# Performance work log

Measured on AMD Instinct MI355X. Metric: run time of the kernel, lower is better.

Reference implementation:

```python
import jax, jax.numpy as jnp
import numpy as np

B, S, D, F, E, K = 4, 2048, 1024, 4096, 8, 2
LBW = 0.01  # load_balance_weight


def setup_inputs() -> dict:
    key = jax.random.key(0)
    ks = jax.random.split(key, 8)
    sd, sf = 1.0 / np.sqrt(D), 1.0 / np.sqrt(F)
    return {
        "x": jax.random.normal(ks[0], (B, S, D), dtype=jnp.float32),
        "expert_weights": jax.random.normal(ks[1], (B, E), dtype=jnp.float32),
        "gate_w": jax.random.uniform(ks[2], (D, E), minval=-sd, maxval=sd),
        "gate_b": jnp.zeros((E,), jnp.float32),
        "w1": jax.random.uniform(ks[3], (E, D, F), minval=-sd, maxval=sd),
        "b1": jnp.zeros((E, F), jnp.float32),
        "w2": jax.random.uniform(ks[4], (E, F, D), minval=-sf, maxval=sf),
        "b2": jnp.zeros((E, D), jnp.float32),
    }


def reference(x, expert_weights, gate_w, gate_b, w1, b1, w2, b2):
    b, s, d = x.shape
    xf = x.reshape(-1, d)                       # (T, D), T = B*S
    T = xf.shape[0]

    logits = xf @ gate_w + gate_b               # (T, E)
    bias = jnp.broadcast_to(expert_weights[:, None, :], (b, s, E)).reshape(-1, E)
    gate_probs = jax.nn.softmax(logits + bias, axis=-1)

    topk_p, topk_i = jax.lax.top_k(gate_probs, K)
    topk_p = topk_p / topk_p.sum(axis=-1, keepdims=True)

    # combine[t, e] = renormalized routing weight of token t for expert e (0 if unrouted)
    combine = jnp.zeros((T, E), xf.dtype).at[jnp.arange(T)[:, None], topk_i].add(topk_p)

    out = jnp.zeros_like(xf)
    for e in range(E):  # fixed small expert loop; dense per-expert GEMMs (dropout inactive in eval)
        h = jax.nn.gelu(xf @ w1[e] + b1[e], approximate=False)  # torch GELU = exact erf
        out = out + combine[:, e:e + 1] * (h @ w2[e] + b2[e])

    # Switch-style load balance loss
    top1 = jnp.argmax(gate_probs, axis=-1)
    f = jnp.mean(jax.nn.one_hot(top1, E, dtype=gate_probs.dtype), axis=0)
    P = gate_probs.mean(axis=0)
    load_loss = LBW * E * jnp.sum(f * P)

    return out.reshape(b, s, d), load_loss
```

## Files before the change

### kernel.cpp

```cpp
#include <hip/hip_runtime.h>
#include <math.h>

#define B_ 4
#define S_ 2048
#define D_ 1024
#define F_ 4096
#define E_ 8
#define T_ 8192
#define LBW_ 0.01f
#define HROWS_ 17408
#define NTILE_MAX 72

#define BUFB 24576

typedef unsigned short u16;
typedef __attribute__((ext_vector_type(8))) short bf16x8;
typedef __attribute__((ext_vector_type(4))) float f32x4;

#define GLOAD16(gp, lp) __builtin_amdgcn_global_load_lds( \
    (const __attribute__((address_space(1))) void*)(gp),  \
    (__attribute__((address_space(3))) void*)(lp), 16, 0, 0)

__device__ __forceinline__ u16 f2b(float f) {
    unsigned u = __float_as_uint(f);
    u = (u + 0x7FFFu + ((u >> 16) & 1u)) >> 16;
    return (u16)u;
}
__device__ __forceinline__ float gelu_f(float v) {
    return 0.5f * v * (1.0f + erff(v * 0.70710678118654752440f));
}

__global__ __launch_bounds__(256) void cvt_T_kernel(const float* __restrict__ src,
                                                    u16* __restrict__ dst, int R, int C) {
    __shared__ u16 t[64][72];
    const int e = blockIdx.z;
    const float* s = src + (size_t)e * R * C;
    u16* d = dst + (size_t)e * R * C;
    const int r0 = blockIdx.y * 64, c0 = blockIdx.x * 64;
    const int tid = threadIdx.x;
    {
        int rr = tid >> 2, cq = (tid & 3) * 16;
        #pragma unroll
        for (int j = 0; j < 16; j += 4) {
            float4 v = *(const float4*)(s + (size_t)(r0 + rr) * C + c0 + cq + j);
            t[cq + j + 0][rr] = f2b(v.x);
            t[cq + j + 1][rr] = f2b(v.y);
            t[cq + j + 2][rr] = f2b(v.z);
            t[cq + j + 3][rr] = f2b(v.w);
        }
    }
    __syncthreads();
    {
        int cr = tid >> 2, rq = (tid & 3) * 16;
        #pragma unroll
        for (int j = 0; j < 16; j += 8) {
            int4 pk; u16* pw = (u16*)&pk;
            #pragma unroll
            for (int jj = 0; jj < 8; ++jj) pw[jj] = t[cr][rq + j + jj];
            *(int4*)(d + (size_t)(c0 + cr) * R + r0 + rq + j) = pk;
        }
    }
}

__global__ __launch_bounds__(64) void gate_kernel(
    const float* __restrict__ x, const float* __restrict__ ew,
    const float* __restrict__ gw, const float* __restrict__ gb,
    u16* __restrict__ xb,
    float* __restrict__ combine, int* __restrict__ idx, int* __restrict__ cnt,
    int* __restrict__ fcnt, float* __restrict__ psum)
{
    const int t = blockIdx.x, l = threadIdx.x;
    const float* xr = x + (size_t)t * D_;
    double acc[E_];
    #pragma unroll
    for (int e = 0; e < E_; ++e) acc[e] = 0.0;
    u16 xw[16];
    #pragma unroll
    for (int kk = 0; kk < 16; kk += 4) {
        float4 xv = *(const float4*)(xr + l * 16 + kk);
        float xs[4] = {xv.x, xv.y, xv.z, xv.w};
        #pragma unroll
        for (int j = 0; j < 4; ++j) {
            xw[kk + j] = f2b(xs[j]);
            const float* gr = gw + (size_t)(l * 16 + kk + j) * E_;
            float4 g0 = *(const float4*)(gr);
            float4 g1 = *(const float4*)(gr + 4);
            acc[0] += (double)xs[j] * g0.x;  acc[1] += (double)xs[j] * g0.y;
            acc[2] += (double)xs[j] * g0.z;  acc[3] += (double)xs[j] * g0.w;
            acc[4] += (double)xs[j] * g1.x;  acc[5] += (double)xs[j] * g1.y;
            acc[6] += (double)xs[j] * g1.z;  acc[7] += (double)xs[j] * g1.w;
        }
    }
    *(int4*)(xb + (size_t)t * D_ + l * 16)     = *(int4*)(xw);
    *(int4*)(xb + (size_t)t * D_ + l * 16 + 8) = *(int4*)(xw + 8);
    #pragma unroll
    for (int e = 0; e < E_; ++e) {
        #pragma unroll
        for (int m = 32; m > 0; m >>= 1) acc[e] += __shfl_xor(acc[e], m);
    }
    if (l == 0) {
        const int b = t / S_;
        double p[E_]; double mx = -1e300;
        #pragma unroll
        for (int e = 0; e < E_; ++e) {
            p[e] = acc[e] + (double)gb[e] + (double)ew[b * E_ + e];
            mx = fmax(mx, p[e]);
        }
        double s = 0.0;
        #pragma unroll
        for (int e = 0; e < E_; ++e) { p[e] = exp(p[e] - mx); s += p[e]; }
        double inv = 1.0 / s;
        #pragma unroll
        for (int e = 0; e < E_; ++e) p[e] *= inv;
        double m1 = -1.0; int e1 = 0;
        #pragma unroll
        for (int e = 0; e < E_; ++e) if (p[e] > m1) { m1 = p[e]; e1 = e; }
        double m2 = -1.0; int e2 = 0;
        #pragma unroll
        for (int e = 0; e < E_; ++e) if (e != e1 && p[e] > m2) { m2 = p[e]; e2 = e; }
        float c1 = (float)(m1 / (m1 + m2)), c2 = (float)(m2 / (m1 + m2));
        #pragma unroll
        for (int e = 0; e < E_; ++e)
            combine[t * E_ + e] = (e == e1) ? c1 : ((e == e2) ? c2 : 0.0f);
        int q1 = atomicAdd(&cnt[e1], 1); idx[e1 * T_ + q1] = t;
        int q2 = atomicAdd(&cnt[e2], 1); idx[e2 * T_ + q2] = t;
        atomicAdd(&fcnt[(t & 63) * E_ + e1], 1);
        #pragma unroll
        for (int e = 0; e < E_; ++e) atomicAdd(&psum[(t & 63) * E_ + e], (float)p[e]);
    }
}

__global__ void tiletab_kernel(const int* __restrict__ cnt, int* __restrict__ off,
                               int* __restrict__ table, int* __restrict__ ntab) {
    if (threadIdx.x == 0 && blockIdx.x == 0) {
        int o = 0, k = 0;
        for (int e = 0; e < E_; ++e) {
            off[e] = o;
            int pad = ((cnt[e] + 127) >> 7) << 7;
            o += pad;
            int nt = (pad + 255) >> 8;
            for (int i = 0; i < nt; ++i) table[k++] = e | (i << 4);
        }
        off[E_] = o;
        *ntab = k;
    }
}

__global__ __launch_bounds__(256) void gather_kernel(
    const u16* __restrict__ xb, const int* __restrict__ idx,
    const int* __restrict__ cnt, const int* __restrict__ off,
    u16* __restrict__ xg)
{
    const int r = blockIdx.x * 16 + (threadIdx.x >> 4);
    const int total = off[E_];
    if (r >= total) return;
    int e = 0;
    #pragma unroll
    for (int k = 1; k < E_; ++k) if (off[k] <= r) e = k;
    const int loc = r - off[e];
    const int cb = (threadIdx.x & 15) * 8;
    u16* dst = xg + (size_t)r * D_;
    if (loc < cnt[e]) {
        const u16* src = xb + (size_t)idx[e * T_ + loc] * D_;
        #pragma unroll
        for (int j = 0; j < 8; ++j)
            *(int4*)(dst + j * 128 + cb) = *(const int4*)(src + j * 128 + cb);
    } else {
        int4 z = {0, 0, 0, 0};
        #pragma unroll
        for (int j = 0; j < 8; ++j) *(int4*)(dst + j * 128 + cb) = z;
    }
}

template<int NT, int KDROW, int NTN, bool IS_G1>
__global__ __launch_bounds__(512, 4) void moe_gemm2c(
    const u16* __restrict__ Aglob, const u16* __restrict__ Wt,
    const float* __restrict__ bias, const float* __restrict__ combine,
    const int* __restrict__ idxAll, const int* __restrict__ cntAll,
    const int* __restrict__ off, const int* __restrict__ table,
    const int* __restrict__ ntab,
    u16* __restrict__ hOut, float* __restrict__ out)
{
    const int gid = blockIdx.x;
    const int ti = gid % NTILE_MAX;
    const int tn = gid / NTILE_MAX;
    if (ti >= *ntab) return;
    const int ent = table[ti];
    const int e = ent & 15, tm = ent >> 4;
    const int cnt = cntAll[e], base = off[e];
    const int* idx_e = idxAll + e * T_;
    const u16* Bsrc = Wt + (size_t)e * ((size_t)D_ * F_);

    __shared__ __align__(16) char lds[3 * BUFB];

    const int tid = threadIdx.x;
    const int l = tid & 63, wid = tid >> 6;
    const int wm = (wid >> 1) * 64, wn = (wid & 1) * 64;
    const int lr = l & 15, lg = l >> 4;

    const int qsrc = ((l & 3) ^ ((l >> 3) & 3)) * 8;
    const u16* aP[2]; const u16* bP;
    #pragma unroll
    for (int i = 0; i < 2; ++i) {
        int c = 2 * wid + i;
        int hr = base + tm * 256 + c * 16 + (l >> 2);
        if (hr > HROWS_ - 1) hr = HROWS_ - 1;
        aP[i] = Aglob + (size_t)hr * KDROW + qsrc;
    }
    {
        int cc = tn * 128 + wid * 16 + (l >> 2);
        bP = Bsrc + (size_t)cc * KDROW + qsrc;
    }

    f32x4 acc[4][4];
    #pragma unroll
    for (int mi = 0; mi < 4; ++mi)
        #pragma unroll
        for (int ni = 0; ni < 4; ++ni) acc[mi][ni] = (f32x4){0.f,0.f,0.f,0.f};

    auto stage = [&](int sb, int kof) {
        GLOAD16(aP[0] + kof, lds + sb + (2 * wid) * 1024);
        GLOAD16(aP[1] + kof, lds + sb + (2 * wid + 1) * 1024);
        GLOAD16(bP + kof, lds + sb + 16384 + wid * 1024);
    };

    stage(0, 0);
    stage(BUFB, 32);
    asm volatile("s_waitcnt vmcnt(3)" ::: "memory");
    __builtin_amdgcn_s_barrier();

    const int koff = ((((lr >> 1) & 3) ^ lg) << 4);
    int cb = 0, sb2 = 2 * BUFB, kofe = 64;
    for (int t = 0; t < NT; ++t) {
        bf16x8 a[4], b[4];
        #pragma unroll
        for (int mi = 0; mi < 4; ++mi)
            a[mi] = *(const bf16x8*)(lds + cb + (wm + mi * 16 + lr) * 64 + koff);
        #pragma unroll
        for (int ni = 0; ni < 4; ++ni)
            b[ni] = *(const bf16x8*)(lds + cb + 16384 + (wn + ni * 16 + lr) * 64 + koff);
        if (t < NT - 2) { stage(sb2, kofe); kofe += 32; }
        __builtin_amdgcn_s_setprio(1);
        #pragma unroll
        for (int mi = 0; mi < 4; ++mi)
            #pragma unroll
            for (int ni = 0; ni < 4; ++ni)
                acc[mi][ni] = __builtin_amdgcn_mfma_f32_16x16x32_bf16(a[mi], b[ni], acc[mi][ni], 0, 0, 0);
        __builtin_amdgcn_s_setprio(0);
        if (t < NT - 2)       { asm volatile("s_waitcnt vmcnt(3)" ::: "memory"); }
        else if (t == NT - 2) { asm volatile("s_waitcnt vmcnt(0)" ::: "memory"); }
        if (t < NT - 1) __builtin_amdgcn_s_barrier();
        cb += BUFB;  if (cb == 3 * BUFB)  cb = 0;
        sb2 += BUFB; if (sb2 == 3 * BUFB) sb2 = 0;
    }

    if (IS_G1) {
        const float* be = bias + e * F_;
        const int pad = ((cnt + 127) >> 7) << 7;
        #pragma unroll
        for (int mi = 0; mi < 4; ++mi) {
            #pragma unroll
            for (int j = 0; j < 4; ++j) {
                int rl = tm * 256 + wm + mi * 16 + lg * 4 + j;
                if (rl < pad) {
                    size_t srow = (size_t)(base + rl) * F_;
                    #pragma unroll
                    for (int ni = 0; ni < 4; ++ni) {
                        int f = tn * 128 + wn + ni * 16 + lr;
                        hOut[srow + f] = f2b(gelu_f(acc[mi][ni][j] + be[f]));
                    }
                }
            }
        }
    } else {
        const float* be = bias + e * D_;
        #pragma unroll
        for (int mi = 0; mi < 4; ++mi) {
            #pragma unroll
            for (int j = 0; j < 4; ++j) {
                int rl = tm * 256 + wm + mi * 16 + lg * 4 + j;
                if (rl < cnt) {
                    int tkn = idx_e[rl];
                    float cw = combine[tkn * E_ + e];
                    float* orow = out + (size_t)tkn * D_;
                    #pragma unroll
                    for (int ni = 0; ni < 4; ++ni) {
                        int d = tn * 128 + wn + ni * 16 + lr;
                        atomicAdd(&orow[d], cw * (acc[mi][ni][j] + be[d]));
                    }
                }
            }
        }
    }
}

__global__ void loss_kernel(const int* __restrict__ fcnt, const float* __restrict__ psum,
                            float* __restrict__ dst) {
    if (threadIdx.x == 0 && blockIdx.x == 0) {
        float loss = 0.f;
        for (int e = 0; e < E_; ++e) {
            float fs = 0.f, Ps = 0.f;
            for (int s = 0; s < 64; ++s) { fs += (float)fcnt[s * E_ + e]; Ps += psum[s * E_ + e]; }
            loss += (fs / (float)T_) * (Ps / (float)T_);
        }
        *dst = LBW_ * (float)E_ * loss;
    }
}

__global__ void sentinel_kernel(float* __restrict__ dst) {
    if (threadIdx.x == 0) dst[0] = -12345.0f;
}

extern "C" void kernel_launch(void* const* d_in, const int* in_sizes, int n_in,
                              void* d_out, int out_size, void* d_ws, size_t ws_size,
                              hipStream_t stream)
{
    const float* x  = (const float*)d_in[0];
    const float* ew = (const float*)d_in[1];
    const float* gw = (const float*)d_in[2];
    const float* gb = (const float*)d_in[3];
    const float* w1 = (const float*)d_in[4];
    const float* b1 = (const float*)d_in[5];
    const float* w2 = (const float*)d_in[6];
    const float* b2 = (const float*)d_in[7];
    float* out = (float*)d_out;

    char* ws = (char*)d_ws;
    size_t o = 0;
    u16* w1t = (u16*)(ws + o); o += (size_t)E_ * D_ * F_ * 2;
    u16* w2t = (u16*)(ws + o); o += (size_t)E_ * F_ * D_ * 2;
    u16* xb  = (u16*)(ws + o); o += (size_t)T_ * D_ * 2;
    u16* xg  = (u16*)(ws + o); o += (size_t)HROWS_ * D_ * 2;
    u16* h   = (u16*)(ws + o); o += (size_t)HROWS_ * F_ * 2;
    float* combine = (float*)(ws + o); o += (size_t)T_ * E_ * 4;
    int* idx = (int*)(ws + o); o += (size_t)E_ * T_ * 4;
    size_t zoff = o;
    int* cnt   = (int*)(ws + o); o += 128;
    int* fcnt  = (int*)(ws + o); o += 64 * E_ * 4;
    float* psum = (float*)(ws + o); o += 64 * E_ * 4;
    int* off   = (int*)(ws + o); o += 128;
    int* table = (int*)(ws + o); o += 512;
    int* ntab  = (int*)(ws + o); o += 128;
    const size_t ws_needed = o;

    if (ws_size < ws_needed) {
        hipMemsetAsync(d_out, 0, (size_t)out_size * sizeof(float), stream);
        sentinel_kernel<<<1, 64, 0, stream>>>(out + (size_t)out_size - 1);
        return;
    }

    hipMemsetAsync(ws + zoff, 0, ws_needed - zoff, stream);
    hipMemsetAsync(d_out, 0, (size_t)out_size * sizeof(float), stream);

    cvt_T_kernel<<<dim3(F_ / 64, D_ / 64, E_), 256, 0, stream>>>(w1, w1t, D_, F_);
    cvt_T_kernel<<<dim3(D_ / 64, F_ / 64, E_), 256, 0, stream>>>(w2, w2t, F_, D_);
    gate_kernel<<<T_, 64, 0, stream>>>(x, ew, gw, gb, xb, combine, idx, cnt, fcnt, psum);
    tiletab_kernel<<<1, 64, 0, stream>>>(cnt, off, table, ntab);
    gather_kernel<<<HROWS_ / 16, 256, 0, stream>>>(xb, idx, cnt, off, xg);
    moe_gemm2c<32, 1024, 32, true><<<NTILE_MAX * 32, 512, 0, stream>>>(
        xg, w1t, b1, nullptr, idx, cnt, off, table, ntab, h, nullptr);
    moe_gemm2c<128, 4096, 8, false><<<NTILE_MAX * 8, 512, 0, stream>>>(
        h, w2t, b2, combine, idx, cnt, off, table, ntab, nullptr, out);
    loss_kernel<<<1, 64, 0, stream>>>(fcnt, psum, out + (size_t)out_size - 1);
}
```

Measured before the change: 841.6 us.

## Fuse token gather into GEMM1, load GEMM2 A operand from registers, merge loss into tiletab

After: 1.177 ms. 39.8% more time.

```diff
diff --git a/kernel.cpp b/kernel.cpp
--- a/kernel.cpp
+++ b/kernel.cpp
@@ -11,7 +11,7 @@
 #define HROWS_ 17408
 #define NTILE_MAX 72
 
-#define BUFB 24576
+#define BUFB1 24576
 
 typedef unsigned short u16;
 typedef __attribute__((ext_vector_type(8))) short bf16x8;
@@ -131,7 +131,9 @@
 }
 
 __global__ void tiletab_kernel(const int* __restrict__ cnt, int* __restrict__ off,
-                               int* __restrict__ table, int* __restrict__ ntab) {
+                               int* __restrict__ table, int* __restrict__ ntab,
+                               const int* __restrict__ fcnt, const float* __restrict__ psum,
+                               float* __restrict__ lossdst) {
     if (threadIdx.x == 0 && blockIdx.x == 0) {
         int o = 0, k = 0;
         for (int e = 0; e < E_; ++e) {
@@ -143,43 +145,22 @@
         }
         off[E_] = o;
         *ntab = k;
-    }
-}
-
-__global__ __launch_bounds__(256) void gather_kernel(
-    const u16* __restrict__ xb, const int* __restrict__ idx,
-    const int* __restrict__ cnt, const int* __restrict__ off,
-    u16* __restrict__ xg)
-{
-    const int r = blockIdx.x * 16 + (threadIdx.x >> 4);
-    const int total = off[E_];
-    if (r >= total) return;
-    int e = 0;
-    #pragma unroll
-    for (int k = 1; k < E_; ++k) if (off[k] <= r) e = k;
-    const int loc = r - off[e];
-    const int cb = (threadIdx.x & 15) * 8;
-    u16* dst = xg + (size_t)r * D_;
-    if (loc < cnt[e]) {
-        const u16* src = xb + (size_t)idx[e * T_ + loc] * D_;
-        #pragma unroll
-        for (int j = 0; j < 8; ++j)
-            *(int4*)(dst + j * 128 + cb) = *(const int4*)(src + j * 128 + cb);
-    } else {
-        int4 z = {0, 0, 0, 0};
-        #pragma unroll
-        for (int j = 0; j < 8; ++j) *(int4*)(dst + j * 128 + cb) = z;
-    }
-}
-
-template<int NT, int KDROW, int NTN, bool IS_G1>
-__global__ __launch_bounds__(512, 4) void moe_gemm2c(
-    const u16* __restrict__ Aglob, const u16* __restrict__ Wt,
-    const float* __restrict__ bias, const float* __restrict__ combine,
+        float loss = 0.f;
+        for (int e = 0; e < E_; ++e) {
+            float fs = 0.f, Ps = 0.f;
+            for (int s = 0; s < 64; ++s) { fs += (float)fcnt[s * E_ + e]; Ps += psum[s * E_ + e]; }
+            loss += (fs / (float)T_) * (Ps / (float)T_);
+        }
+        *lossdst = LBW_ * (float)E_ * loss;
+    }
+}
+
+__global__ __launch_bounds__(512, 4) void moe_g1_kernel(
+    const u16* __restrict__ xb, const u16* __restrict__ Wt,
+    const float* __restrict__ bias,
     const int* __restrict__ idxAll, const int* __restrict__ cntAll,
     const int* __restrict__ off, const int* __restrict__ table,
-    const int* __restrict__ ntab,
-    u16* __restrict__ hOut, float* __restrict__ out)
+    const int* __restrict__ ntab, u16* __restrict__ hOut)
 {
     const int gid = blockIdx.x;
     const int ti = gid % NTILE_MAX;
@@ -191,7 +172,7 @@
     const int* idx_e = idxAll + e * T_;
     const u16* Bsrc = Wt + (size_t)e * ((size_t)D_ * F_);
 
-    __shared__ __align__(16) char lds[3 * BUFB];
+    __shared__ __align__(16) char lds[3 * BUFB1];
 
     const int tid = threadIdx.x;
     const int l = tid & 63, wid = tid >> 6;
@@ -203,13 +184,13 @@
     #pragma unroll
     for (int i = 0; i < 2; ++i) {
         int c = 2 * wid + i;
-        int hr = base + tm * 256 + c * 16 + (l >> 2);
-        if (hr > HROWS_ - 1) hr = HROWS_ - 1;
-        aP[i] = Aglob + (size_t)hr * KDROW + qsrc;
+        int r = tm * 256 + c * 16 + (l >> 2);
+        int tok = (r < cnt) ? idx_e[r] : idx_e[0];
+        aP[i] = xb + (size_t)tok * D_ + qsrc;
     }
     {
         int cc = tn * 128 + wid * 16 + (l >> 2);
-        bP = Bsrc + (size_t)cc * KDROW + qsrc;
+        bP = Bsrc + (size_t)cc * D_ + qsrc;
     }
 
     f32x4 acc[4][4];
@@ -225,12 +206,13 @@
     };
 
     stage(0, 0);
-    stage(BUFB, 32);
+    stage(BUFB1, 32);
     asm volatile("s_waitcnt vmcnt(3)" ::: "memory");
     __builtin_amdgcn_s_barrier();
 
     const int koff = ((((lr >> 1) & 3) ^ lg) << 4);
-    int cb = 0, sb2 = 2 * BUFB, kofe = 64;
+    int cb = 0, sb2 = 2 * BUFB1, kofe = 64;
+    constexpr int NT = 32;
     for (int t = 0; t < NT; ++t) {
         bf16x8 a[4], b[4];
         #pragma unroll
@@ -250,60 +232,139 @@
         if (t < NT - 2)       { asm volatile("s_waitcnt vmcnt(3)" ::: "memory"); }
         else if (t == NT - 2) { asm volatile("s_waitcnt vmcnt(0)" ::: "memory"); }
         if (t < NT - 1) __builtin_amdgcn_s_barrier();
-        cb += BUFB;  if (cb == 3 * BUFB)  cb = 0;
-        sb2 += BUFB; if (sb2 == 3 * BUFB) sb2 = 0;
-    }
-
-    if (IS_G1) {
-        const float* be = bias + e * F_;
-        const int pad = ((cnt + 127) >> 7) << 7;
-        #pragma unroll
-        for (int mi = 0; mi < 4; ++mi) {
-            #pragma unroll
-            for (int j = 0; j < 4; ++j) {
-                int rl = tm * 256 + wm + mi * 16 + lg * 4 + j;
-                if (rl < pad) {
-                    size_t srow = (size_t)(base + rl) * F_;
-                    #pragma unroll
-                    for (int ni = 0; ni < 4; ++ni) {
-                        int f = tn * 128 + wn + ni * 16 + lr;
-                        hOut[srow + f] = f2b(gelu_f(acc[mi][ni][j] + be[f]));
-                    }
+        cb += BUFB1;  if (cb == 3 * BUFB1)  cb = 0;
+        sb2 += BUFB1; if (sb2 == 3 * BUFB1) sb2 = 0;
+    }
+
+    const float* be = bias + e * F_;
+    const int pad = ((cnt + 127) >> 7) << 7;
+    #pragma unroll
+    for (int mi = 0; mi < 4; ++mi) {
+        #pragma unroll
+        for (int j = 0; j < 4; ++j) {
+            int rl = tm * 256 + wm + mi * 16 + lg * 4 + j;
+            if (rl < pad) {
+                size_t srow = (size_t)(base + rl) * F_;
+                #pragma unroll
+                for (int ni = 0; ni < 4; ++ni) {
+                    int f = tn * 128 + wn + ni * 16 + lr;
+                    hOut[srow + f] = f2b(gelu_f(acc[mi][ni][j] + be[f]));
                 }
             }
         }
-    } else {
-        const float* be = bias + e * D_;
-        #pragma unroll
-        for (int mi = 0; mi < 4; ++mi) {
-            #pragma unroll
-            for (int j = 0; j < 4; ++j) {
-                int rl = tm * 256 + wm + mi * 16 + lg * 4 + j;
-                if (rl < cnt) {
-                    int tkn = idx_e[rl];
-                    float cw = combine[tkn * E_ + e];
-                    float* orow = out + (size_t)tkn * D_;
-                    #pragma unroll
-                    for (int ni = 0; ni < 4; ++ni) {
-                        int d = tn * 128 + wn + ni * 16 + lr;
-                        atomicAdd(&orow[d], cw * (acc[mi][ni][j] + be[d]));
-                    }
+    }
+}
+
+__global__ __launch_bounds__(512, 4) void moe_g2_kernel(
+    const u16* __restrict__ h, const u16* __restrict__ Wt,
+    const float* __restrict__ bias, const float* __restrict__ combine,
+    const int* __restrict__ idxAll, const int* __restrict__ cntAll,
+    const int* __restrict__ off, const int* __restrict__ table,
+    const int* __restrict__ ntab, float* __restrict__ out)
+{
+    const int gid = blockIdx.x;
+    const int ti = gid % NTILE_MAX;
+    const int tn = gid / NTILE_MAX;
+    if (ti >= *ntab) return;
+    const int ent = table[ti];
+    const int e = ent & 15, tm = ent >> 4;
+    const int cnt = cntAll[e], base = off[e];
+    const int* idx_e = idxAll + e * T_;
+    const u16* Bsrc = Wt + (size_t)e * ((size_t)D_ * F_);
+
+    __shared__ __align__(16) char lds[3 * 8192];
+
+    const int tid = threadIdx.x;
+    const int l = tid & 63, wid = tid >> 6;
+    const int wm = (wid >> 1) * 64, wn = (wid & 1) * 64;
+    const int lr = l & 15, lg = l >> 4;
+    constexpr int NT = 128;
+
+    const int qsrc = ((l & 3) ^ ((l >> 3) & 3)) * 8;
+    const u16* bP;
+    {
+        int cc = tn * 128 + wid * 16 + (l >> 2);
+        bP = Bsrc + (size_t)cc * F_ + qsrc;
+    }
+    const u16* aRow[4];
+    #pragma unroll
+    for (int mi = 0; mi < 4; ++mi) {
+        int hr = base + tm * 256 + wm + mi * 16 + lr;
+        if (hr > HROWS_ - 1) hr = HROWS_ - 1;
+        aRow[mi] = h + (size_t)hr * F_ + lg * 8;
+    }
+
+    f32x4 acc[4][4];
+    #pragma unroll
+    for (int mi = 0; mi < 4; ++mi)
+        #pragma unroll
+        for (int ni = 0; ni < 4; ++ni) acc[mi][ni] = (f32x4){0.f,0.f,0.f,0.f};
+
+    bf16x8 aA[4], aB[4];
+    GLOAD16(bP + 0,  lds + 0 * 8192 + wid * 1024);
+    GLOAD16(bP + 32, lds + 1 * 8192 + wid * 1024);
+    #pragma unroll
+    for (int mi = 0; mi < 4; ++mi) aA[mi] = *(const bf16x8*)(aRow[mi]);
+    #pragma unroll
+    for (int mi = 0; mi < 4; ++mi) aB[mi] = *(const bf16x8*)(aRow[mi] + 32);
+    asm volatile("s_waitcnt vmcnt(9)" ::: "memory");
+    __builtin_amdgcn_s_barrier();
+
+    const int koff = ((((lr >> 1) & 3) ^ lg) << 4);
+
+#define G2_TILE(AV, TEXPR)                                                      \
+    {                                                                           \
+        const int t = (TEXPR);                                                  \
+        const char* Bb = lds + (t % 3) * 8192;                                  \
+        bf16x8 b[4];                                                            \
+        _Pragma("unroll")                                                       \
+        for (int ni = 0; ni < 4; ++ni)                                          \
+            b[ni] = *(const bf16x8*)(Bb + (wn + ni * 16 + lr) * 64 + koff);     \
+        if (t < NT - 2)                                                         \
+            GLOAD16(bP + (t + 2) * 32, lds + ((t + 2) % 3) * 8192 + wid * 1024);\
+        __builtin_amdgcn_s_setprio(1);                                          \
+        _Pragma("unroll")                                                       \
+        for (int mi = 0; mi < 4; ++mi)                                          \
+            _Pragma("unroll")                                                   \
+            for (int ni = 0; ni < 4; ++ni)                                      \
+                acc[mi][ni] = __builtin_amdgcn_mfma_f32_16x16x32_bf16(          \
+                    AV[mi], b[ni], acc[mi][ni], 0, 0, 0);                       \
+        __builtin_amdgcn_s_setprio(0);                                          \
+        if (t < NT - 2) {                                                       \
+            _Pragma("unroll")                                                   \
+            for (int mi = 0; mi < 4; ++mi)                                      \
+                AV[mi] = *(const bf16x8*)(aRow[mi] + (t + 2) * 32);             \
+            asm volatile("s_waitcnt vmcnt(5)" ::: "memory");                    \
+        } else if (t == NT - 2) {                                               \
+            asm volatile("s_waitcnt vmcnt(0)" ::: "memory");                    \
+        }                                                                       \
+        if (t < NT - 1) __builtin_amdgcn_s_barrier();                           \
+    }
+
+    #pragma unroll 1
+    for (int t2 = 0; t2 < NT / 2; ++t2) {
+        G2_TILE(aA, 2 * t2);
+        G2_TILE(aB, 2 * t2 + 1);
+    }
+#undef G2_TILE
+
+    const float* be = bias + e * D_;
+    #pragma unroll
+    for (int mi = 0; mi < 4; ++mi) {
+        #pragma unroll
+        for (int j = 0; j < 4; ++j) {
+            int rl = tm * 256 + wm + mi * 16 + lg * 4 + j;
+            if (rl < cnt) {
+                int tkn = idx_e[rl];
+                float cw = combine[tkn * E_ + e];
+                float* orow = out + (size_t)tkn * D_;
+                #pragma unroll
+                for (int ni = 0; ni < 4; ++ni) {
+                    int d = tn * 128 + wn + ni * 16 + lr;
+                    atomicAdd(&orow[d], cw * (acc[mi][ni][j] + be[d]));
                 }
             }
         }
-    }
-}
-
-__global__ void loss_kernel(const int* __restrict__ fcnt, const float* __restrict__ psum,
-                            float* __restrict__ dst) {
-    if (threadIdx.x == 0 && blockIdx.x == 0) {
-        float loss = 0.f;
-        for (int e = 0; e < E_; ++e) {
-            float fs = 0.f, Ps = 0.f;
-            for (int s = 0; s < 64; ++s) { fs += (float)fcnt[s * E_ + e]; Ps += psum[s * E_ + e]; }
-            loss += (fs / (float)T_) * (Ps / (float)T_);
-        }
-        *dst = LBW_ * (float)E_ * loss;
     }
 }
 
@@ -330,7 +391,6 @@
     u16* w1t = (u16*)(ws + o); o += (size_t)E_ * D_ * F_ * 2;
     u16* w2t = (u16*)(ws + o); o += (size_t)E_ * F_ * D_ * 2;
     u16* xb  = (u16*)(ws + o); o += (size_t)T_ * D_ * 2;
-    u16* xg  = (u16*)(ws + o); o += (size_t)HROWS_ * D_ * 2;
     u16* h   = (u16*)(ws + o); o += (size_t)HROWS_ * F_ * 2;
     float* combine = (float*)(ws + o); o += (size_t)T_ * E_ * 4;
     int* idx = (int*)(ws + o); o += (size_t)E_ * T_ * 4;
@@ -344,22 +404,21 @@
     const size_t ws_needed = o;
 
     if (ws_size < ws_needed) {
-        hipMemsetAsync(d_out, 0, (size_t)out_size * sizeof(float), stream);
+        (void)hipMemsetAsync(d_out, 0, (size_t)out_size * sizeof(float), stream);
         sentinel_kernel<<<1, 64, 0, stream>>>(out + (size_t)out_size - 1);
         return;
     }
 
-    hipMemsetAsync(ws + zoff, 0, ws_needed - zoff, stream);
-    hipMemsetAsync(d_out, 0, (size_t)out_size * sizeof(float), stream);
+    (void)hipMemsetAsync(ws + zoff, 0, ws_needed - zoff, stream);
+    (void)hipMemsetAsync(d_out, 0, (size_t)out_size * sizeof(float), stream);
 
     cvt_T_kernel<<<dim3(F_ / 64, D_ / 64, E_), 256, 0, stream>>>(w1, w1t, D_, F_);
     cvt_T_kernel<<<dim3(D_ / 64, F_ / 64, E_), 256, 0, stream>>>(w2, w2t, F_, D_);
     gate_kernel<<<T_, 64, 0, stream>>>(x, ew, gw, gb, xb, combine, idx, cnt, fcnt, psum);
-    tiletab_kernel<<<1, 64, 0, stream>>>(cnt, off, table, ntab);
-    gather_kernel<<<HROWS_ / 16, 256, 0, stream>>>(xb, idx, cnt, off, xg);
-    moe_gemm2c<32, 1024, 32, true><<<NTILE_MAX * 32, 512, 0, stream>>>(
-        xg, w1t, b1, nullptr, idx, cnt, off, table, ntab, h, nullptr);
-    moe_gemm2c<128, 4096, 8, false><<<NTILE_MAX * 8, 512, 0, stream>>>(
-        h, w2t, b2, combine, idx, cnt, off, table, ntab, nullptr, out);
-    loss_kernel<<<1, 64, 0, stream>>>(fcnt, psum, out + (size_t)out_size - 1);
-}
+    tiletab_kernel<<<1, 64, 0, stream>>>(cnt, off, table, ntab, fcnt, psum,
+                                         out + (size_t)out_size - 1);
+    moe_g1_kernel<<<NTILE_MAX * 32, 512, 0, stream>>>(
+        xb, w1t, b1, idx, cnt, off, table, ntab, h);
+    moe_g2_kernel<<<NTILE_MAX * 8, 512, 0, stream>>>(
+        h, w2t, b2, combine, idx, cnt, off, table, ntab, out);
+}
```

## Fuse gather into GEMM1 loads, merge weight converts and loss into existing kernels

Applied to the files above, without the earlier changes.

Result: faster. 805.5 us (-4.3%).

```diff
diff --git a/kernel.cpp b/kernel.cpp
--- a/kernel.cpp
+++ b/kernel.cpp
@@ -30,13 +30,21 @@
     return 0.5f * v * (1.0f + erff(v * 0.70710678118654752440f));
 }
 
-__global__ __launch_bounds__(256) void cvt_T_kernel(const float* __restrict__ src,
-                                                    u16* __restrict__ dst, int R, int C) {
+__global__ __launch_bounds__(256) void cvt_both_kernel(const float* __restrict__ w1,
+                                                       const float* __restrict__ w2,
+                                                       u16* __restrict__ w1t,
+                                                       u16* __restrict__ w2t) {
     __shared__ u16 t[64][72];
-    const int e = blockIdx.z;
-    const float* s = src + (size_t)e * R * C;
-    u16* d = dst + (size_t)e * R * C;
-    const int r0 = blockIdx.y * 64, c0 = blockIdx.x * 64;
+    const int bid = blockIdx.x;
+    const int w = bid >> 13;
+    const int r2 = bid & 8191;
+    const int e = r2 >> 10, cell = r2 & 1023;
+    const int R = w ? F_ : D_, C = w ? D_ : F_;
+    const int bx = w ? (cell & 15) : (cell & 63);
+    const int by = w ? (cell >> 4) : (cell >> 6);
+    const float* s = (w ? w2 : w1) + (size_t)e * D_ * F_;
+    u16* d = (w ? w2t : w1t) + (size_t)e * D_ * F_;
+    const int r0 = by * 64, c0 = bx * 64;
     const int tid = threadIdx.x;
     {
         int rr = tid >> 2, cq = (tid & 3) * 16;
@@ -131,7 +139,9 @@
 }
 
 __global__ void tiletab_kernel(const int* __restrict__ cnt, int* __restrict__ off,
-                               int* __restrict__ table, int* __restrict__ ntab) {
+                               int* __restrict__ table, int* __restrict__ ntab,
+                               const int* __restrict__ fcnt, const float* __restrict__ psum,
+                               float* __restrict__ lossdst) {
     if (threadIdx.x == 0 && blockIdx.x == 0) {
         int o = 0, k = 0;
         for (int e = 0; e < E_; ++e) {
@@ -143,37 +153,18 @@
         }
         off[E_] = o;
         *ntab = k;
-    }
-}
-
-__global__ __launch_bounds__(256) void gather_kernel(
-    const u16* __restrict__ xb, const int* __restrict__ idx,
-    const int* __restrict__ cnt, const int* __restrict__ off,
-    u16* __restrict__ xg)
-{
-    const int r = blockIdx.x * 16 + (threadIdx.x >> 4);
-    const int total = off[E_];
-    if (r >= total) return;
-    int e = 0;
-    #pragma unroll
-    for (int k = 1; k < E_; ++k) if (off[k] <= r) e = k;
-    const int loc = r - off[e];
-    const int cb = (threadIdx.x & 15) * 8;
-    u16* dst = xg + (size_t)r * D_;
-    if (loc < cnt[e]) {
-        const u16* src = xb + (size_t)idx[e * T_ + loc] * D_;
-        #pragma unroll
-        for (int j = 0; j < 8; ++j)
-            *(int4*)(dst + j * 128 + cb) = *(const int4*)(src + j * 128 + cb);
-    } else {
-        int4 z = {0, 0, 0, 0};
-        #pragma unroll
-        for (int j = 0; j < 8; ++j) *(int4*)(dst + j * 128 + cb) = z;
-    }
-}
-
-template<int NT, int KDROW, int NTN, bool IS_G1>
-__global__ __launch_bounds__(512, 4) void moe_gemm2c(
+        float loss = 0.f;
+        for (int e = 0; e < E_; ++e) {
+            float fs = 0.f, Ps = 0.f;
+            for (int s = 0; s < 64; ++s) { fs += (float)fcnt[s * E_ + e]; Ps += psum[s * E_ + e]; }
+            loss += (fs / (float)T_) * (Ps / (float)T_);
+        }
+        *lossdst = LBW_ * (float)E_ * loss;
+    }
+}
+
+template<int NT, int KDROW, bool IS_G1>
+__global__ __launch_bounds__(512, 4) void moe_gemm_kernel(
     const u16* __restrict__ Aglob, const u16* __restrict__ Wt,
     const float* __restrict__ bias, const float* __restrict__ combine,
     const int* __restrict__ idxAll, const int* __restrict__ cntAll,
@@ -203,9 +194,14 @@
     #pragma unroll
     for (int i = 0; i < 2; ++i) {
         int c = 2 * wid + i;
-        int hr = base + tm * 256 + c * 16 + (l >> 2);
-        if (hr > HROWS_ - 1) hr = HROWS_ - 1;
-        aP[i] = Aglob + (size_t)hr * KDROW + qsrc;
+        int r = tm * 256 + c * 16 + (l >> 2);
+        if (IS_G1) {
+            int tok = (r < cnt) ? idx_e[r] : idx_e[0];
+            aP[i] = Aglob + (size_t)tok * KDROW + qsrc;
+        } else {
+            int hr = base + r; if (hr > HROWS_ - 1) hr = HROWS_ - 1;
+            aP[i] = Aglob + (size_t)hr * KDROW + qsrc;
+        }
     }
     {
         int cc = tn * 128 + wid * 16 + (l >> 2);
@@ -294,19 +290,6 @@
     }
 }
 
-__global__ void loss_kernel(const int* __restrict__ fcnt, const float* __restrict__ psum,
-                            float* __restrict__ dst) {
-    if (threadIdx.x == 0 && blockIdx.x == 0) {
-        float loss = 0.f;
-        for (int e = 0; e < E_; ++e) {
-            float fs = 0.f, Ps = 0.f;
-            for (int s = 0; s < 64; ++s) { fs += (float)fcnt[s * E_ + e]; Ps += psum[s * E_ + e]; }
-            loss += (fs / (float)T_) * (Ps / (float)T_);
-        }
-        *dst = LBW_ * (float)E_ * loss;
-    }
-}
-
 __global__ void sentinel_kernel(float* __restrict__ dst) {
     if (threadIdx.x == 0) dst[0] = -12345.0f;
 }
@@ -330,7 +313,6 @@
     u16* w1t = (u16*)(ws + o); o += (size_t)E_ * D_ * F_ * 2;
     u16* w2t = (u16*)(ws + o); o += (size_t)E_ * F_ * D_ * 2;
     u16* xb  = (u16*)(ws + o); o += (size_t)T_ * D_ * 2;
-    u16* xg  = (u16*)(ws + o); o += (size_t)HROWS_ * D_ * 2;
     u16* h   = (u16*)(ws + o); o += (size_t)HROWS_ * F_ * 2;
     float* combine = (float*)(ws + o); o += (size_t)T_ * E_ * 4;
     int* idx = (int*)(ws + o); o += (size_t)E_ * T_ * 4;
@@ -344,22 +326,20 @@
     const size_t ws_needed = o;
 
     if (ws_size < ws_needed) {
-        hipMemsetAsync(d_out, 0, (size_t)out_size * sizeof(float), stream);
+        (void)hipMemsetAsync(d_out, 0, (size_t)out_size * sizeof(float), stream);
         sentinel_kernel<<<1, 64, 0, stream>>>(out + (size_t)out_size - 1);
         return;
     }
 
-    hipMemsetAsync(ws + zoff, 0, ws_needed - zoff, stream);
-    hipMemsetAsync(d_out, 0, (size_t)out_size * sizeof(float), stream);
-
-    cvt_T_kernel<<<dim3(F_ / 64, D_ / 64, E_), 256, 0, stream>>>(w1, w1t, D_, F_);
-    cvt_T_kernel<<<dim3(D_ / 64, F_ / 64, E_), 256, 0, stream>>>(w2, w2t, F_, D_);
+    (void)hipMemsetAsync(ws + zoff, 0, ws_needed - zoff, stream);
+    (void)hipMemsetAsync(d_out, 0, (size_t)out_size * sizeof(float), stream);
+
+    cvt_both_kernel<<<16384, 256, 0, stream>>>(w1, w2, w1t, w2t);
     gate_kernel<<<T_, 64, 0, stream>>>(x, ew, gw, gb, xb, combine, idx, cnt, fcnt, psum);
-    tiletab_kernel<<<1, 64, 0, stream>>>(cnt, off, table, ntab);
-    gather_kernel<<<HROWS_ / 16, 256, 0, stream>>>(xb, idx, cnt, off, xg);
-    moe_gemm2c<32, 1024, 32, true><<<NTILE_MAX * 32, 512, 0, stream>>>(
-        xg, w1t, b1, nullptr, idx, cnt, off, table, ntab, h, nullptr);
-    moe_gemm2c<128, 4096, 8, false><<<NTILE_MAX * 8, 512, 0, stream>>>(
+    tiletab_kernel<<<1, 64, 0, stream>>>(cnt, off, table, ntab, fcnt, psum,
+                                         out + (size_t)out_size - 1);
+    moe_gemm_kernel<32, 1024, true><<<NTILE_MAX * 32, 512, 0, stream>>>(
+        xb, w1t, b1, nullptr, idx, cnt, off, table, ntab, h, nullptr);
+    moe_gemm_kernel<128, 4096, false><<<NTILE_MAX * 8, 512, 0, stream>>>(
         h, w2t, b2, combine, idx, cnt, off, table, ntab, nullptr, out);
-    loss_kernel<<<1, 64, 0, stream>>>(fcnt, psum, out + (size_t)out_size - 1);
-}
+}
```
